# Kernel tuning notes

Measured on AMD Instinct MI355X. Metric: run time of the kernel, lower is better.

## Reference

```python
import jax, jax.numpy as jnp
import numpy as np

N, E = 50000, 500000          # nodes, edges
IN_DIM = 128
HID = 128
T, R, H, L = 4, 5, 4, 2       # node types, edge types, heads, layers
DK = HID // H                 # per-head dim


def setup_inputs() -> dict:
    key = jax.random.key(0)
    ks = jax.random.split(key, 16)
    s = 0.05
    inp = {
        "node_feature": jax.random.normal(ks[0], (N, IN_DIM), jnp.float32),
        "node_type": jax.random.randint(ks[1], (N,), 0, T, jnp.int32),
        "edge_time": jax.random.randint(ks[2], (E,), 0, 128, jnp.int32),
        "edge_index": jax.random.randint(ks[3], (2, E), 0, N, jnp.int32),
        "edge_type": jax.random.randint(ks[4], (E,), 0, R, jnp.int32),
        # per-node-type input adaptation
        "adapt_w": jax.random.normal(ks[5], (T, IN_DIM, HID), jnp.float32) * s,
        "adapt_b": jnp.zeros((T, HID), jnp.float32),
        # HGT layer params, stacked over layers L and node types T
        "kw": jax.random.normal(ks[6], (L, T, HID, HID), jnp.float32) * s,
        "kb": jnp.zeros((L, T, HID), jnp.float32),
        "qw": jax.random.normal(ks[7], (L, T, HID, HID), jnp.float32) * s,
        "qb": jnp.zeros((L, T, HID), jnp.float32),
        "vw": jax.random.normal(ks[8], (L, T, HID, HID), jnp.float32) * s,
        "vb": jnp.zeros((L, T, HID), jnp.float32),
        "aw": jax.random.normal(ks[9], (L, T, HID, HID), jnp.float32) * s,
        "ab": jnp.zeros((L, T, HID), jnp.float32),
        # relation (edge-type) specific params
        "rel_pri": jnp.ones((L, R, H), jnp.float32),
        "rel_att": jax.random.normal(ks[10], (L, R, H, DK, DK), jnp.float32) * (1.0 / np.sqrt(DK)),
        "rel_msg": jax.random.normal(ks[11], (L, R, H, DK, DK), jnp.float32) * (1.0 / np.sqrt(DK)),
        "skip": jnp.ones((L, T), jnp.float32),
    }
    return inp


def _type_linear(x, types, W, b):
    # per-node-type linear: small fixed loop over T types, masked select
    out = jnp.zeros((x.shape[0], W.shape[-1]), x.dtype)
    for t in range(W.shape[0]):
        out = jnp.where((types == t)[:, None], x @ W[t] + b[t], out)
    return out


def _hgt_layer(x, node_type, src, dst, edge_type,
               kw, kb, qw, qb, vw, vb, aw, ab, rel_pri, rel_att, rel_msg, skip):
    n = x.shape[0]
    k = _type_linear(x, node_type, kw, kb).reshape(n, H, DK)
    q = _type_linear(x, node_type, qw, qb).reshape(n, H, DK)
    v = _type_linear(x, node_type, vw, vb).reshape(n, H, DK)
    ke, qe, ve = k[src], q[dst], v[src]              # [E,H,DK] gathers
    att = jnp.zeros((ke.shape[0], H), x.dtype)
    msg = jnp.zeros_like(ve)
    inv_sqrt_dk = np.float32(1.0 / np.sqrt(DK))
    for r in range(R):                                # small fixed loop over edge types
        m = edge_type == r
        kt = jnp.einsum('ehi,hij->ehj', ke, rel_att[r])
        a = (qe * kt).sum(-1) * rel_pri[r] * inv_sqrt_dk   # [E,H]
        mt = jnp.einsum('ehi,hij->ehj', ve, rel_msg[r])    # [E,H,DK]
        att = jnp.where(m[:, None], a, att)
        msg = jnp.where(m[:, None, None], mt, msg)
    # segment softmax over incoming edges of each destination node
    amax = jax.ops.segment_max(att, dst, num_segments=n)
    amax = jnp.where(jnp.isfinite(amax), amax, 0.0)
    ex = jnp.exp(att - amax[dst])
    den = jax.ops.segment_sum(ex, dst, num_segments=n)
    alpha = ex / jnp.maximum(den[dst], 1e-9)
    res = jax.ops.segment_sum(alpha[:, :, None] * msg, dst, num_segments=n).reshape(n, HID)
    # target-specific update with gated residual (HGT skip)
    trans = _type_linear(jax.nn.gelu(res), node_type, aw, ab)
    sk = jax.nn.sigmoid(skip)[node_type][:, None]
    return trans * sk + x * (1.0 - sk)


def reference(node_feature, node_type, edge_time, edge_index, edge_type,
              adapt_w, adapt_b, kw, kb, qw, qb, vw, vb, aw, ab,
              rel_pri, rel_att, rel_msg, skip):
    # per-type adapt -> tanh (dropout p=0 is identity)
    h = jnp.tanh(_type_linear(node_feature, node_type, adapt_w, adapt_b))
    src, dst = edge_index[0], edge_index[1]
    for l in range(L):
        h = _hgt_layer(h, node_type, src, dst, edge_type,
                       kw[l], kb[l], qw[l], qb[l], vw[l], vb[l], aw[l], ab[l],
                       rel_pri[l], rel_att[l], rel_msg[l], skip[l])
    return h
```

## Files before the change

### kernel.cpp

```cpp
#include <hip/hip_runtime.h>

#define T_NT 4
#define T_R  5
#define T_H  4
#define T_DK 32
#define T_HD 128
#define T_L  2
#define NCOL 1408

typedef unsigned short u16;
typedef __bf16 bf8_t __attribute__((ext_vector_type(8)));
typedef float f4_t __attribute__((ext_vector_type(4)));

__device__ __forceinline__ float bf2f(u16 u){
  union { float f; unsigned int i; } v; v.i = ((unsigned int)u) << 16; return v.f;
}
__device__ __forceinline__ float blo(unsigned u){
  union { float f; unsigned int i; } v; v.i = u << 16; return v.f;
}
__device__ __forceinline__ float bhi(unsigned u){
  union { float f; unsigned int i; } v; v.i = u & 0xffff0000u; return v.f;
}
__device__ __forceinline__ u16 f2bf(float f){
  union { float f; unsigned int i; } v; v.f = f;
  unsigned int x = v.i;
  return (u16)((x + 0x7fffu + ((x >> 16) & 1u)) >> 16);
}
__device__ __forceinline__ unsigned pk2(float a, float b){
  return (unsigned)f2bf(a) | ((unsigned)f2bf(b) << 16);
}
__device__ __forceinline__ float gelu_f(float x){
  float x3 = x*x*x;
  return 0.5f * x * (1.f + tanhf(0.7978845608028654f * (x + 0.044715f * x3)));
}
__device__ __forceinline__ int perm_l(int m){
  return (m & ~31) | ((m & 4) << 2) | ((m & 24) >> 1) | (m & 3);
}

__global__ void k_hist4(const int* __restrict__ key, int* __restrict__ cnt, int n){
  __shared__ int c[T_NT];
  int tid = threadIdx.x;
  if (tid < T_NT) c[tid] = 0;
  __syncthreads();
  int base = blockIdx.x*1024;
#pragma unroll
  for (int j=0;j<4;j++){
    int i = base + tid + j*256;
    if (i < n) atomicAdd(&c[key[i]], 1);
  }
  __syncthreads();
  if (tid < T_NT) atomicAdd(&cnt[tid], c[tid]);
}

__global__ void k_toff(const int* __restrict__ cnt, int* __restrict__ off, int* __restrict__ tcur){
  if (threadIdx.x == 0){
    off[0] = 0;
    for (int t = 0; t < T_NT; ++t) off[t+1] = off[t] + cnt[t];
    for (int t = 0; t < T_NT; ++t) tcur[t] = off[t];
  }
}

__global__ void k_scatter2(const int* __restrict__ nt, int* __restrict__ tcur,
                           int* __restrict__ perm, int* __restrict__ iperm, int n){
  __shared__ int lc[T_NT], lb[T_NT];
  int tid = threadIdx.x;
  if (tid < T_NT) lc[tid] = 0;
  __syncthreads();
  int base = blockIdx.x*1024;
  int t[4], lr[4];
#pragma unroll
  for (int j=0;j<4;j++){
    int i = base + tid + j*256;
    if (i < n){ t[j] = nt[i]; lr[j] = atomicAdd(&lc[t[j]], 1); }
    else t[j] = -1;
  }
  __syncthreads();
  if (tid < T_NT) lb[tid] = atomicAdd(&tcur[tid], lc[tid]);
  __syncthreads();
#pragma unroll
  for (int j=0;j<4;j++){
    if (t[j] >= 0){
      int node = base + tid + j*256;
      int pos = lb[t[j]] + lr[j];
      perm[pos] = node;
      iperm[node] = pos;
    }
  }
}

__global__ void k_deg(const int* __restrict__ dstp, const int* __restrict__ iperm,
                      int* __restrict__ degp, int* __restrict__ rank, int n){
  int i = blockIdx.x*256 + threadIdx.x;
  if (i < n) rank[i] = atomicAdd(&degp[(size_t)iperm[dstp[i]] << 4], 1);
}

__global__ void k_scanA(const int* __restrict__ degp, int* __restrict__ rp,
                        int* __restrict__ bsum, int n){
  __shared__ int buf[256];
  int tid = threadIdx.x;
  int i = blockIdx.x*256 + tid;
  int v = (i < n) ? degp[(size_t)i << 4] : 0;
  buf[tid] = v;
  __syncthreads();
  for (int off = 1; off < 256; off <<= 1){
    int add = (tid >= off) ? buf[tid - off] : 0;
    __syncthreads();
    buf[tid] += add;
    __syncthreads();
  }
  if (i < n) rp[i] = buf[tid] - v;
  if (tid == 255) bsum[blockIdx.x] = buf[255];
}
__global__ void k_scanB(int* __restrict__ bsum, int nb){
  __shared__ int buf[1024];
  int tid = threadIdx.x;
  int v = (tid < nb) ? bsum[tid] : 0;
  buf[tid] = v;
  __syncthreads();
  for (int off = 1; off < 1024; off <<= 1){
    int add = (tid >= off) ? buf[tid - off] : 0;
    __syncthreads();
    buf[tid] += add;
    __syncthreads();
  }
  if (tid < nb) bsum[tid] = buf[tid] - v;
}
__global__ void k_scanC(int* __restrict__ rp, const int* __restrict__ bsum,
                        int n, int E){
  int i = blockIdx.x*256 + threadIdx.x;
  if (i < n) rp[i] += bsum[blockIdx.x];
  if (i == 0) rp[n] = E;
}

__global__ void k_fill2(const int* __restrict__ srcp, const int* __restrict__ dstp,
                        const int* __restrict__ etp, const int* __restrict__ iperm,
                        const int* __restrict__ rp, const int* __restrict__ rank,
                        int* __restrict__ packed, int n){
  int i = blockIdx.x*256 + threadIdx.x;
  if (i < n){
    int d = iperm[dstp[i]];
    packed[rp[d] + rank[i]] = iperm[srcp[i]] | (etp[i] << 17);
  }
}

__global__ void k_prepmisc(const float* __restrict__ kw, const float* __restrict__ kb,
                           const float* __restrict__ qb, const float* __restrict__ vb,
                           const float* __restrict__ rel_att, const float* __restrict__ rel_msg,
                           const float* __restrict__ rel_pri,
                           u16* __restrict__ Ball, float* __restrict__ biasall)
{
  const float isd = 0.17677669529663687f;
  int idx = blockIdx.x*256 + threadIdx.x;
  if (idx < T_L*T_NT*T_HD*T_HD){
    int col = idx & 127, k = (idx >> 7) & 127, lt = idx >> 14;
    Ball[((size_t)lt*NCOL + col)*T_HD + k] = f2bf(kw[((size_t)lt*T_HD + k)*T_HD + col]);
    if (k == 0) biasall[(size_t)lt*NCOL + col] = kb[(size_t)lt*T_HD + col];
    return;
  }
  int b = idx - T_L*T_NT*T_HD*T_HD;
  if (b >= T_L*T_NT*1280) return;
  int lt = b / 1280, cc = b % 1280;
  int l = lt >> 2;
  int qv = cc >= 640, rem = cc - qv*640;
  int r = rem >> 7, hd = rem & 127, h = hd >> 5, o = hd & 31;
  float s = 0.f;
  if (!qv){
    const float* Ar = rel_att + ((((size_t)l*T_R + r)*T_H + h)*T_DK + o)*T_DK;
    const float* qbr = qb + (size_t)lt*T_HD + h*T_DK;
#pragma unroll
    for (int j = 0; j < 32; ++j) s += qbr[j] * Ar[j];
    s *= rel_pri[((size_t)l*T_R + r)*T_H + h] * isd;
  } else {
    const float* Mr = rel_msg + (((size_t)l*T_R + r)*T_H + h)*T_DK*T_DK + o;
    const float* vbr = vb + (size_t)lt*T_HD + h*T_DK;
#pragma unroll
    for (int i = 0; i < 32; ++i) s += vbr[i] * Mr[i*T_DK];
  }
  biasall[(size_t)lt*NCOL + 128 + qv*640 + r*128 + h*32 + o] = s;
}

__global__ __launch_bounds__(256)
void k_prepqv(const float* __restrict__ qw, const float* __restrict__ vw,
              const float* __restrict__ rel_att, const float* __restrict__ rel_msg,
              const float* __restrict__ rel_pri, u16* __restrict__ Ball)
{
  __shared__ float Ws[T_HD*33];
  __shared__ float As_[T_R*32*36];
  const float isd = 0.17677669529663687f;
  int h = blockIdx.x & 3, qv = blockIdx.x >> 2;
  int t = blockIdx.y, l = blockIdx.z;
  int lt = l*T_NT + t;
  int tid = threadIdx.x;
  const float* W = (qv ? vw : qw) + (size_t)lt*T_HD*T_HD;
  const float* rel = (qv ? rel_msg : rel_att);
#pragma unroll
  for (int i = 0; i < 16; ++i){
    int idx = tid + i*256;
    int j = idx & 31, k = idx >> 5;
    Ws[k*33 + j] = W[(size_t)k*T_HD + h*T_DK + j];
  }
#pragma unroll
  for (int i = 0; i < 20; ++i){
    int idx = tid + i*256;
    int bcol = idx & 31, a = (idx >> 5) & 31, r = idx >> 10;
    float wv = rel[((((size_t)l*T_R + r)*T_H + h)*T_DK + a)*T_DK + bcol];
    if (qv) As_[r*1152 + bcol*36 + a] = wv;
    else    As_[r*1152 + a*36 + bcol] = wv;
  }
  __syncthreads();
  int k = tid & 127, io = tid >> 7;
  float Wrow[32];
#pragma unroll
  for (int c = 0; c < 32; ++c) Wrow[c] = Ws[k*33 + c];
  for (int r = 0; r < T_R; ++r){
    float scale = qv ? 1.f : rel_pri[((size_t)l*T_R + r)*T_H + h] * isd;
#pragma unroll
    for (int i2 = 0; i2 < 16; ++i2){
      int o = i2*2 + io;
      const float4* ap = (const float4*)&As_[r*1152 + o*36];
      float acc = 0.f;
#pragma unroll
      for (int c4 = 0; c4 < 8; ++c4){
        float4 a4 = ap[c4];
        acc += Wrow[c4*4+0]*a4.x + Wrow[c4*4+1]*a4.y + Wrow[c4*4+2]*a4.z + Wrow[c4*4+3]*a4.w;
      }
      int col = 128 + qv*640 + r*128 + h*32 + o;
      Ball[((size_t)lt*NCOL + col)*T_HD + k] = f2bf(acc*scale);
    }
  }
}

__global__ __launch_bounds__(256)
void k_qkvm(const float* __restrict__ X, const int* __restrict__ toff,
            const u16* __restrict__ Ball, const float* __restrict__ biasall,
            u16* __restrict__ kB, u16* __restrict__ qt, u16* __restrict__ mtp)
{
  __shared__ u16 As[64*128];
  int t = blockIdx.y;
  int z = blockIdx.z;
  int lo = toff[t], cnt = toff[t+1] - lo;
  int base = (int)blockIdx.x * 64;
  if (base >= cnt) return;
  int tid = threadIdx.x;
#pragma unroll
  for (int it = 0; it < 4; ++it){
    int chunk = tid + it*256;
    int row = chunk >> 4, c8 = (chunk & 15) << 3;
    uint4 o = make_uint4(0,0,0,0);
    if (base + row < cnt){
      const float* src = X + (size_t)(lo + base + row)*T_HD + c8;
      float4 f0 = *(const float4*)src;
      float4 f1 = *(const float4*)(src + 4);
      o.x = pk2(f0.x, f0.y);
      o.y = pk2(f0.z, f0.w);
      o.z = pk2(f1.x, f1.y);
      o.w = pk2(f1.z, f1.w);
    }
    int off16 = (row*128 + c8) ^ ((row & 7) << 3);
    *(uint4*)&As[off16] = o;
  }
  __syncthreads();

  int wid = tid >> 6, lane = tid & 63;
  int lr = lane & 15, lg = lane >> 4;
  bf8_t a[4][4];
#pragma unroll
  for (int rs = 0; rs < 4; ++rs)
#pragma unroll
    for (int kk = 0; kk < 4; ++kk){
      int row = rs*16 + lr;
      int off16 = (row*128 + kk*32 + lg*8) ^ ((row & 7) << 3);
      a[rs][kk] = *(const bf8_t*)&As[off16];
    }

  const u16* Bt = Ball + (size_t)t * NCOL * T_HD;
  const float* biast = biasall + (size_t)t * NCOL;

  int ci_end = z ? 44 : 22;
  for (int ci = z*22 + wid; ci < ci_end; ci += 4){
    int c0 = ci*2;
    int col0 = c0*16 + lr;
    const u16* bp0 = Bt + (size_t)col0*T_HD + lg*8;
    const u16* bp1 = bp0 + (size_t)16*T_HD;
    bf8_t b00 = *(const bf8_t*)(bp0);
    bf8_t b01 = *(const bf8_t*)(bp0 + 32);
    bf8_t b02 = *(const bf8_t*)(bp0 + 64);
    bf8_t b03 = *(const bf8_t*)(bp0 + 96);
    bf8_t b10 = *(const bf8_t*)(bp1);
    bf8_t b11 = *(const bf8_t*)(bp1 + 32);
    bf8_t b12 = *(const bf8_t*)(bp1 + 64);
    bf8_t b13 = *(const bf8_t*)(bp1 + 96);
    f4_t acc0[4], acc1[4];
#pragma unroll
    for (int rs = 0; rs < 4; ++rs){ acc0[rs] = (f4_t){0.f,0.f,0.f,0.f}; acc1[rs] = (f4_t){0.f,0.f,0.f,0.f}; }
#pragma unroll
    for (int rs = 0; rs < 4; ++rs){
      acc0[rs] = __builtin_amdgcn_mfma_f32_16x16x32_bf16(b00, a[rs][0], acc0[rs], 0, 0, 0);
      acc0[rs] = __builtin_amdgcn_mfma_f32_16x16x32_bf16(b01, a[rs][1], acc0[rs], 0, 0, 0);
      acc0[rs] = __builtin_amdgcn_mfma_f32_16x16x32_bf16(b02, a[rs][2], acc0[rs], 0, 0, 0);
      acc0[rs] = __builtin_amdgcn_mfma_f32_16x16x32_bf16(b03, a[rs][3], acc0[rs], 0, 0, 0);
      acc1[rs] = __builtin_amdgcn_mfma_f32_16x16x32_bf16(b10, a[rs][0], acc1[rs], 0, 0, 0);
      acc1[rs] = __builtin_amdgcn_mfma_f32_16x16x32_bf16(b11, a[rs][1], acc1[rs], 0, 0, 0);
      acc1[rs] = __builtin_amdgcn_mfma_f32_16x16x32_bf16(b12, a[rs][2], acc1[rs], 0, 0, 0);
      acc1[rs] = __builtin_amdgcn_mfma_f32_16x16x32_bf16(b13, a[rs][3], acc1[rs], 0, 0, 0);
    }
    float4 bias0 = *(const float4*)&biast[c0*16 + lg*4];
    float4 bias1 = *(const float4*)&biast[c0*16 + 16 + lg*4];
    int mco = ci*32 + lg*8;
    u16* dst; int cofs, stride;
    if (ci < 4)       { dst = kB;  cofs = mco;        stride = T_HD; }
    else if (ci < 24) { dst = qt;  cofs = mco - 128;  stride = T_R*T_HD; }
    else              { dst = mtp; cofs = mco - 768;  stride = T_R*T_HD; }
#pragma unroll
    for (int rs = 0; rs < 4; ++rs){
      int nl = rs*16 + lr;
      if (base + nl < cnt){
        uint4 o;
        o.x = pk2(acc0[rs][0] + bias0.x, acc0[rs][1] + bias0.y);
        o.y = pk2(acc0[rs][2] + bias0.z, acc0[rs][3] + bias0.w);
        o.z = pk2(acc1[rs][0] + bias1.x, acc1[rs][1] + bias1.y);
        o.w = pk2(acc1[rs][2] + bias1.z, acc1[rs][3] + bias1.w);
        *(uint4*)&dst[(size_t)(lo + base + nl)*stride + cofs] = o;
      }
    }
  }
}

template<int MODE, int GIN, int SOUT>
__global__ __launch_bounds__(256)
void k_typed_gemm(const float* __restrict__ X,
                  const int* __restrict__ tperm, const int* __restrict__ toff,
                  const float* __restrict__ W, const float* __restrict__ Bi,
                  float* __restrict__ outv,
                  const float* __restrict__ h_in, const float* __restrict__ skipv)
{
  int t = blockIdx.y;
  int lo = toff[t], cnt = toff[t+1] - lo;
  int base = (int)blockIdx.x * 64;
  if (base >= cnt) return;
  __shared__ float As[64][16];
  __shared__ float Bs[16][128];
  __shared__ int rows_s[64];
  int tid = threadIdx.x;
  if (GIN || SOUT){
    if (tid < 64) rows_s[tid] = (base + tid < cnt) ? tperm[lo + base + tid] : -1;
    __syncthreads();
  }
  float acc[8][4];
#pragma unroll
  for (int i=0;i<8;i++){ acc[i][0]=0.f;acc[i][1]=0.f;acc[i][2]=0.f;acc[i][3]=0.f; }
  int ty = tid >> 5, tx = tid & 31;
  const float* Wt = W + (size_t)t * (T_HD*T_HD);
  for (int k0 = 0; k0 < T_HD; k0 += 16){
#pragma unroll
    for (int j=0;j<4;j++){
      int idx = tid + j*256;
      int m = idx >> 4, kk = idx & 15;
      float v = 0.f;
      if (base + m < cnt){
        if (GIN){
          int row = rows_s[m];
          v = X[(size_t)row*T_HD + k0 + kk];
        } else {
          v = X[(size_t)(lo + base + m)*T_HD + k0 + kk];
        }
        if (MODE == 3) v = gelu_f(v);
      }
      As[m][kk] = v;
    }
#pragma unroll
    for (int j=0;j<8;j++){
      int idx = tid + j*256;
      int kk = idx >> 7, c = idx & 127;
      int kg = k0 + kk;
      if (MODE == 3) kg = perm_l(kg);
      Bs[kk][c] = Wt[(size_t)kg*T_HD + c];
    }
    __syncthreads();
#pragma unroll
    for (int kk=0;kk<16;kk++){
      float4 bv = *(const float4*)&Bs[kk][tx*4];
#pragma unroll
      for (int i=0;i<8;i++){
        float a = As[ty*8+i][kk];
        acc[i][0] += a*bv.x; acc[i][1] += a*bv.y; acc[i][2] += a*bv.z; acc[i][3] += a*bv.w;
      }
    }
    __syncthreads();
  }
  float sk = 0.f;
  if (MODE == 3) sk = 1.f / (1.f + __expf(-skipv[t]));
#pragma unroll
  for (int i=0;i<8;i++){
    int m = ty*8 + i;
    if (base + m >= cnt) continue;
    size_t opos = SOUT ? (size_t)rows_s[m] : (size_t)(lo + base + m);
#pragma unroll
    for (int q=0;q<4;q++){
      int c = tx*4 + q;
      float vv = acc[i][q] + Bi[t*T_HD + c];
      if (MODE == 1) vv = tanhf(vv);
      if (MODE == 3) vv = vv*sk + h_in[(size_t)(lo + base + m)*T_HD + c]*(1.f - sk);
      outv[opos*T_HD + c] = vv;
    }
  }
}

__global__ __launch_bounds__(256)
void k_edge_attn2(const u16* __restrict__ kB, const u16* __restrict__ qt,
                  const u16* __restrict__ mtp, const int* __restrict__ rp,
                  const int* __restrict__ packed, float* __restrict__ resb, int n)
{
  int lane = threadIdx.x & 63;
  int wid = (int)blockIdx.x * (blockDim.x >> 6) + (threadIdx.x >> 6);
  int nw = (int)gridDim.x * (blockDim.x >> 6);
  int l2 = lane << 1;
  for (int dst = wid; dst < n; dst += nw){
    int e0 = rp[dst], e1 = rp[dst+1];
    if (e0 == e1){
      *(float2*)&resb[(size_t)dst*T_HD + l2] = make_float2(0.f, 0.f);
      continue;
    }
    const u16* qrow = qt + (size_t)dst*(T_R*T_HD) + l2;
    float mA=-INFINITY, dA=0.f, aA0=0.f, aA1=0.f;
    float mB=-INFINITY, dB=0.f, aB0=0.f, aB1=0.f;
    int ei = e0;
    for (; ei + 1 < e1; ei += 2){
      int pka = packed[ei], pkb = packed[ei+1];
      int sa = pka & 131071, ra = pka >> 17;
      int sb = pkb & 131071, rb = pkb >> 17;
      unsigned ka = *(const unsigned*)&kB[(sa << 7) + l2];
      unsigned kb = *(const unsigned*)&kB[(sb << 7) + l2];
      unsigned qa = *(const unsigned*)&qrow[ra << 7];
      unsigned qb = *(const unsigned*)&qrow[rb << 7];
      unsigned ma = *(const unsigned*)&mtp[((sa*T_R + ra) << 7) + l2];
      unsigned mb = *(const unsigned*)&mtp[((sb*T_R + rb) << 7) + l2];
      float pa = blo(qa)*blo(ka) + bhi(qa)*bhi(ka);
      float pb = blo(qb)*blo(kb) + bhi(qb)*bhi(kb);
      pa += __shfl_xor(pa, 1);  pb += __shfl_xor(pb, 1);
      pa += __shfl_xor(pa, 2);  pb += __shfl_xor(pb, 2);
      pa += __shfl_xor(pa, 4);  pb += __shfl_xor(pb, 4);
      pa += __shfl_xor(pa, 8);  pb += __shfl_xor(pb, 8);
      float mnA = fmaxf(mA, pa), mnB = fmaxf(mB, pb);
      float scA = __expf(mA - mnA), scB = __expf(mB - mnB);
      float wA = __expf(pa - mnA),  wB = __expf(pb - mnB);
      mA = mnA; mB = mnB;
      dA  = dA*scA + wA;          dB  = dB*scB + wB;
      aA0 = aA0*scA + wA*blo(ma); aB0 = aB0*scB + wB*blo(mb);
      aA1 = aA1*scA + wA*bhi(ma); aB1 = aB1*scB + wB*bhi(mb);
    }
    if (ei < e1){
      int pka = packed[ei];
      int sa = pka & 131071, ra = pka >> 17;
      unsigned ka = *(const unsigned*)&kB[(sa << 7) + l2];
      unsigned qa = *(const unsigned*)&qrow[ra << 7];
      unsigned ma = *(const unsigned*)&mtp[((sa*T_R + ra) << 7) + l2];
      float pa = blo(qa)*blo(ka) + bhi(qa)*bhi(ka);
      pa += __shfl_xor(pa, 1);
      pa += __shfl_xor(pa, 2);
      pa += __shfl_xor(pa, 4);
      pa += __shfl_xor(pa, 8);
      float mnA = fmaxf(mA, pa);
      float scA = __expf(mA - mnA);
      float wA = __expf(pa - mnA);
      mA = mnA;
      dA  = dA*scA + wA;
      aA0 = aA0*scA + wA*blo(ma);
      aA1 = aA1*scA + wA*bhi(ma);
    }
    float mn = fmaxf(mA, mB);
    float eA = __expf(mA - mn), eB = __expf(mB - mn);
    float d  = dA*eA + dB*eB;
    float a0 = aA0*eA + aB0*eB;
    float a1 = aA1*eA + aB1*eB;
    float inv = 1.f / fmaxf(d, 1e-9f);
    *(float2*)&resb[(size_t)dst*T_HD + l2] = make_float2(a0*inv, a1*inv);
  }
}

extern "C" void kernel_launch(void* const* d_in, const int* in_sizes, int n_in,
                              void* d_out, int out_size, void* d_ws, size_t ws_size,
                              hipStream_t stream)
{
  const float* node_feature = (const float*)d_in[0];
  const int* node_type    = (const int*)d_in[1];
  const int* edge_index   = (const int*)d_in[3];
  const int* edge_type    = (const int*)d_in[4];
  const float* adapt_w = (const float*)d_in[5];
  const float* adapt_b = (const float*)d_in[6];
  const float* kw = (const float*)d_in[7];
  const float* kb = (const float*)d_in[8];
  const float* qw = (const float*)d_in[9];
  const float* qb = (const float*)d_in[10];
  const float* vw = (const float*)d_in[11];
  const float* vb = (const float*)d_in[12];
  const float* aw = (const float*)d_in[13];
  const float* ab = (const float*)d_in[14];
  const float* rel_pri = (const float*)d_in[15];
  const float* rel_att = (const float*)d_in[16];
  const float* rel_msg = (const float*)d_in[17];
  const float* skipp   = (const float*)d_in[18];

  const int N = in_sizes[1];
  const int E = in_sizes[4];
  const int* srcp = edge_index;
  const int* dstp = edge_index + E;

  char* p = (char*)d_ws;
  auto take = [&](size_t bytes)->char*{
    char* r = p; p += (bytes + 255) & ~(size_t)255; return r;
  };
  float* h0   = (float*)take((size_t)N*T_HD*4);
  float* resb = (float*)take((size_t)N*T_HD*4);
  u16*  kB    = (u16*) take((size_t)N*T_HD*2);
  u16*  qt    = (u16*) take((size_t)N*T_R*T_HD*2);
  u16*  mtp   = (u16*) take((size_t)N*T_R*T_HD*2);
  u16*  Ball  = (u16*) take((size_t)T_L*T_NT*NCOL*T_HD*2);
  float* biasall = (float*)take((size_t)T_L*T_NT*NCOL*4);
  int* degp   = (int*) take((size_t)N*16*4);
  int* rp     = (int*) take(((size_t)N+1)*4);
  int* rank   = (int*) take((size_t)E*4);
  int* packed = (int*) take((size_t)E*4);
  int* tcnt   = (int*) take(256);
  int* toff   = (int*) take(256);
  int* tcur   = (int*) take(256);
  int* bsum   = (int*) take(1024);
  int* tperm  = (int*) take((size_t)N*4);
  int* iperm  = (int*) take((size_t)N*4);

  hipMemsetAsync(degp, 0, (size_t)N*16*4, stream);
  hipMemsetAsync(tcnt, 0, 256, stream);

  int nb_n4 = (N + 1023)/1024, nb_e = (E + 255)/256;
  int nb_s  = (N + 255)/256;
  k_hist4<<<nb_n4, 256, 0, stream>>>(node_type, tcnt, N);
  k_toff<<<1, 64, 0, stream>>>(tcnt, toff, tcur);
  k_scatter2<<<nb_n4, 256, 0, stream>>>(node_type, tcur, tperm, iperm, N);
  k_deg<<<nb_e, 256, 0, stream>>>(dstp, iperm, degp, rank, E);
  k_scanA<<<nb_s, 256, 0, stream>>>(degp, rp, bsum, N);
  k_scanB<<<1, 1024, 0, stream>>>(bsum, nb_s);
  k_scanC<<<nb_s, 256, 0, stream>>>(rp, bsum, N, E);
  k_fill2<<<nb_e, 256, 0, stream>>>(srcp, dstp, edge_type, iperm, rp, rank, packed, E);

  int misc_total = T_L*T_NT*T_HD*T_HD + T_L*T_NT*1280;
  k_prepmisc<<<(misc_total + 255)/256, 256, 0, stream>>>(
      kw, kb, qb, vb, rel_att, rel_msg, rel_pri, Ball, biasall);
  k_prepqv<<<dim3(8, T_NT, T_L), 256, 0, stream>>>(
      qw, vw, rel_att, rel_msg, rel_pri, Ball);

  dim3 gg((N + 63)/64, T_NT);
  dim3 gq((N + 63)/64, T_NT, 2);
  k_typed_gemm<1,1,0><<<gg, 256, 0, stream>>>(node_feature, tperm, toff, adapt_w, adapt_b, h0, nullptr, nullptr);

  for (int l = 0; l < T_L; ++l){
    size_t wo = (size_t)l * T_NT * T_HD * T_HD;
    size_t bo = (size_t)l * T_NT * T_HD;
    k_qkvm<<<gq, 256, 0, stream>>>(h0, toff,
        Ball + (size_t)l*T_NT*NCOL*T_HD, biasall + (size_t)l*T_NT*NCOL,
        kB, qt, mtp);
    k_edge_attn2<<<2048, 256, 0, stream>>>(kB, qt, mtp, rp, packed, resb, N);
    if (l == T_L - 1)
      k_typed_gemm<3,0,1><<<gg, 256, 0, stream>>>(resb, tperm, toff, aw+wo, ab+bo,
          (float*)d_out, h0, skipp + l*T_NT);
    else
      k_typed_gemm<3,0,0><<<gg, 256, 0, stream>>>(resb, tperm, toff, aw+wo, ab+bo,
          h0, h0, skipp + l*T_NT);
  }
}
```

Before: 460.6 us.

## Replace fp32 typed GEMMs with bf16 MFMA kernels using pre-transposed weights

The per-type adapt and output GEMMs move from scalar fp32 shared-memory tiling to bf16 MFMA 16x16x32 instructions. A new prep kernel converts adapt_w and aw to transposed bf16 and folds the row permutation into the aw copy. The activation tile is staged once in swizzled LDS as bf16, so the k-loop and its barriers disappear. This cuts FMA issue cost on three small GEMMs but lowers input and weight precision to bf16 and adds one prep launch.

```diff
diff --git a/kernel.cpp b/kernel.cpp
--- a/kernel.cpp
+++ b/kernel.cpp
@@ -227,6 +227,21 @@
       int col = 128 + qv*640 + r*128 + h*32 + o;
       Ball[((size_t)lt*NCOL + col)*T_HD + k] = f2bf(acc*scale);
     }
+  }
+}
+
+__global__ void k_prepw2(const float* __restrict__ adapt_w, const float* __restrict__ aw,
+                         u16* __restrict__ adaptT, u16* __restrict__ awT)
+{
+  int idx = blockIdx.x*256 + threadIdx.x;
+  if (idx < T_NT*T_HD*T_HD){
+    int k = idx & 127, col = (idx >> 7) & 127, t = idx >> 14;
+    adaptT[idx] = f2bf(adapt_w[((size_t)t*T_HD + k)*T_HD + col]);
+  } else {
+    int j = idx - T_NT*T_HD*T_HD;
+    if (j >= T_L*T_NT*T_HD*T_HD) return;
+    int k = j & 127, col = (j >> 7) & 127, lt = j >> 14;
+    awT[j] = f2bf(aw[((size_t)lt*T_HD + perm_l(k))*T_HD + col]);
   }
 }
 
@@ -328,80 +343,103 @@
 
 template<int MODE, int GIN, int SOUT>
 __global__ __launch_bounds__(256)
-void k_typed_gemm(const float* __restrict__ X,
-                  const int* __restrict__ tperm, const int* __restrict__ toff,
-                  const float* __restrict__ W, const float* __restrict__ Bi,
-                  float* __restrict__ outv,
-                  const float* __restrict__ h_in, const float* __restrict__ skipv)
+void k_ffn(const float* __restrict__ X, const int* __restrict__ tperm,
+           const int* __restrict__ toff, const u16* __restrict__ WT,
+           const float* __restrict__ Bi, float* __restrict__ outv,
+           const float* __restrict__ h_in, const float* __restrict__ skipv)
 {
+  __shared__ u16 As[64*128];
+  __shared__ int rows_s[64];
   int t = blockIdx.y;
   int lo = toff[t], cnt = toff[t+1] - lo;
   int base = (int)blockIdx.x * 64;
   if (base >= cnt) return;
-  __shared__ float As[64][16];
-  __shared__ float Bs[16][128];
-  __shared__ int rows_s[64];
   int tid = threadIdx.x;
   if (GIN || SOUT){
-    if (tid < 64) rows_s[tid] = (base + tid < cnt) ? tperm[lo + base + tid] : -1;
+    if (tid < 64) rows_s[tid] = (base + tid < cnt) ? tperm[lo + base + tid] : 0;
     __syncthreads();
   }
-  float acc[8][4];
-#pragma unroll
-  for (int i=0;i<8;i++){ acc[i][0]=0.f;acc[i][1]=0.f;acc[i][2]=0.f;acc[i][3]=0.f; }
-  int ty = tid >> 5, tx = tid & 31;
-  const float* Wt = W + (size_t)t * (T_HD*T_HD);
-  for (int k0 = 0; k0 < T_HD; k0 += 16){
-#pragma unroll
-    for (int j=0;j<4;j++){
-      int idx = tid + j*256;
-      int m = idx >> 4, kk = idx & 15;
-      float v = 0.f;
-      if (base + m < cnt){
-        if (GIN){
-          int row = rows_s[m];
-          v = X[(size_t)row*T_HD + k0 + kk];
-        } else {
-          v = X[(size_t)(lo + base + m)*T_HD + k0 + kk];
-        }
-        if (MODE == 3) v = gelu_f(v);
+#pragma unroll
+  for (int it = 0; it < 4; ++it){
+    int chunk = tid + it*256;
+    int row = chunk >> 4, c8 = (chunk & 15) << 3;
+    uint4 o = make_uint4(0,0,0,0);
+    if (base + row < cnt){
+      const float* src = GIN ? (X + (size_t)rows_s[row]*T_HD + c8)
+                             : (X + (size_t)(lo + base + row)*T_HD + c8);
+      float4 f0 = *(const float4*)src;
+      float4 f1 = *(const float4*)(src + 4);
+      if (MODE == 3){
+        f0.x = gelu_f(f0.x); f0.y = gelu_f(f0.y); f0.z = gelu_f(f0.z); f0.w = gelu_f(f0.w);
+        f1.x = gelu_f(f1.x); f1.y = gelu_f(f1.y); f1.z = gelu_f(f1.z); f1.w = gelu_f(f1.w);
       }
-      As[m][kk] = v;
-    }
-#pragma unroll
-    for (int j=0;j<8;j++){
-      int idx = tid + j*256;
-      int kk = idx >> 7, c = idx & 127;
-      int kg = k0 + kk;
-      if (MODE == 3) kg = perm_l(kg);
-      Bs[kk][c] = Wt[(size_t)kg*T_HD + c];
-    }
-    __syncthreads();
-#pragma unroll
-    for (int kk=0;kk<16;kk++){
-      float4 bv = *(const float4*)&Bs[kk][tx*4];
-#pragma unroll
-      for (int i=0;i<8;i++){
-        float a = As[ty*8+i][kk];
-        acc[i][0] += a*bv.x; acc[i][1] += a*bv.y; acc[i][2] += a*bv.z; acc[i][3] += a*bv.w;
-      }
-    }
-    __syncthreads();
-  }
+      o.x = pk2(f0.x, f0.y);
+      o.y = pk2(f0.z, f0.w);
+      o.z = pk2(f1.x, f1.y);
+      o.w = pk2(f1.z, f1.w);
+    }
+    int off16 = (row*128 + c8) ^ ((row & 7) << 3);
+    *(uint4*)&As[off16] = o;
+  }
+  __syncthreads();
+
+  int wid = tid >> 6, lane = tid & 63;
+  int lr = lane & 15, lg = lane >> 4;
+  bf8_t a[4][4];
+#pragma unroll
+  for (int rs = 0; rs < 4; ++rs)
+#pragma unroll
+    for (int kk = 0; kk < 4; ++kk){
+      int row = rs*16 + lr;
+      int off16 = (row*128 + kk*32 + lg*8) ^ ((row & 7) << 3);
+      a[rs][kk] = *(const bf8_t*)&As[off16];
+    }
+
+  const u16* Wt = WT + (size_t)t * T_HD * T_HD;
   float sk = 0.f;
   if (MODE == 3) sk = 1.f / (1.f + __expf(-skipv[t]));
-#pragma unroll
-  for (int i=0;i<8;i++){
-    int m = ty*8 + i;
-    if (base + m >= cnt) continue;
-    size_t opos = SOUT ? (size_t)rows_s[m] : (size_t)(lo + base + m);
-#pragma unroll
-    for (int q=0;q<4;q++){
-      int c = tx*4 + q;
-      float vv = acc[i][q] + Bi[t*T_HD + c];
-      if (MODE == 1) vv = tanhf(vv);
-      if (MODE == 3) vv = vv*sk + h_in[(size_t)(lo + base + m)*T_HD + c]*(1.f - sk);
-      outv[opos*T_HD + c] = vv;
+
+  for (int c = wid; c < 8; c += 4){
+    const u16* bp = Wt + (size_t)(c*16 + lr)*T_HD + lg*8;
+    bf8_t b0 = *(const bf8_t*)(bp);
+    bf8_t b1 = *(const bf8_t*)(bp + 32);
+    bf8_t b2 = *(const bf8_t*)(bp + 64);
+    bf8_t b3 = *(const bf8_t*)(bp + 96);
+    f4_t acc[4];
+#pragma unroll
+    for (int rs = 0; rs < 4; ++rs) acc[rs] = (f4_t){0.f,0.f,0.f,0.f};
+#pragma unroll
+    for (int rs = 0; rs < 4; ++rs){
+      acc[rs] = __builtin_amdgcn_mfma_f32_16x16x32_bf16(b0, a[rs][0], acc[rs], 0, 0, 0);
+      acc[rs] = __builtin_amdgcn_mfma_f32_16x16x32_bf16(b1, a[rs][1], acc[rs], 0, 0, 0);
+      acc[rs] = __builtin_amdgcn_mfma_f32_16x16x32_bf16(b2, a[rs][2], acc[rs], 0, 0, 0);
+      acc[rs] = __builtin_amdgcn_mfma_f32_16x16x32_bf16(b3, a[rs][3], acc[rs], 0, 0, 0);
+    }
+    int cc = c*16 + lg*4;
+    float4 bias4 = *(const float4*)&Bi[t*T_HD + cc];
+#pragma unroll
+    for (int rs = 0; rs < 4; ++rs){
+      int nl = rs*16 + lr;
+      if (base + nl < cnt){
+        float4 vv;
+        vv.x = acc[rs][0] + bias4.x;
+        vv.y = acc[rs][1] + bias4.y;
+        vv.z = acc[rs][2] + bias4.z;
+        vv.w = acc[rs][3] + bias4.w;
+        if (MODE == 1){
+          vv.x = tanhf(vv.x); vv.y = tanhf(vv.y); vv.z = tanhf(vv.z); vv.w = tanhf(vv.w);
+        }
+        if (MODE == 3){
+          float4 hr = *(const float4*)&h_in[(size_t)(lo + base + nl)*T_HD + cc];
+          float osk = 1.f - sk;
+          vv.x = vv.x*sk + hr.x*osk;
+          vv.y = vv.y*sk + hr.y*osk;
+          vv.z = vv.z*sk + hr.z*osk;
+          vv.w = vv.w*sk + hr.w*osk;
+        }
+        size_t opos = SOUT ? (size_t)rows_s[nl] : (size_t)(lo + base + nl);
+        *(float4*)&outv[opos*T_HD + cc] = vv;
+      }
     }
   }
 }
@@ -517,6 +555,8 @@
   u16*  mtp   = (u16*) take((size_t)N*T_R*T_HD*2);
   u16*  Ball  = (u16*) take((size_t)T_L*T_NT*NCOL*T_HD*2);
   float* biasall = (float*)take((size_t)T_L*T_NT*NCOL*4);
+  u16*  adaptT = (u16*)take((size_t)T_NT*T_HD*T_HD*2);
+  u16*  awT    = (u16*)take((size_t)T_L*T_NT*T_HD*T_HD*2);
   int* degp   = (int*) take((size_t)N*16*4);
   int* rp     = (int*) take(((size_t)N+1)*4);
   int* rank   = (int*) take((size_t)E*4);
@@ -547,23 +587,24 @@
       kw, kb, qb, vb, rel_att, rel_msg, rel_pri, Ball, biasall);
   k_prepqv<<<dim3(8, T_NT, T_L), 256, 0, stream>>>(
       qw, vw, rel_att, rel_msg, rel_pri, Ball);
+  int w2_total = T_NT*T_HD*T_HD + T_L*T_NT*T_HD*T_HD;
+  k_prepw2<<<(w2_total + 255)/256, 256, 0, stream>>>(adapt_w, aw, adaptT, awT);
 
   dim3 gg((N + 63)/64, T_NT);
   dim3 gq((N + 63)/64, T_NT, 2);
-  k_typed_gemm<1,1,0><<<gg, 256, 0, stream>>>(node_feature, tperm, toff, adapt_w, adapt_b, h0, nullptr, nullptr);
+  k_ffn<1,1,0><<<gg, 256, 0, stream>>>(node_feature, tperm, toff, adaptT, adapt_b, h0, nullptr, nullptr);
 
   for (int l = 0; l < T_L; ++l){
-    size_t wo = (size_t)l * T_NT * T_HD * T_HD;
     size_t bo = (size_t)l * T_NT * T_HD;
     k_qkvm<<<gq, 256, 0, stream>>>(h0, toff,
         Ball + (size_t)l*T_NT*NCOL*T_HD, biasall + (size_t)l*T_NT*NCOL,
         kB, qt, mtp);
     k_edge_attn2<<<2048, 256, 0, stream>>>(kB, qt, mtp, rp, packed, resb, N);
     if (l == T_L - 1)
-      k_typed_gemm<3,0,1><<<gg, 256, 0, stream>>>(resb, tperm, toff, aw+wo, ab+bo,
-          (float*)d_out, h0, skipp + l*T_NT);
+      k_ffn<3,0,1><<<gg, 256, 0, stream>>>(resb, tperm, toff,
+          awT + (size_t)l*T_NT*T_HD*T_HD, ab + bo, (float*)d_out, h0, skipp + l*T_NT);
     else
-      k_typed_gemm<3,0,0><<<gg, 256, 0, stream>>>(resb, tperm, toff, aw+wo, ab+bo,
-          h0, h0, skipp + l*T_NT);
-  }
-}
+      k_ffn<3,0,0><<<gg, 256, 0, stream>>>(resb, tperm, toff,
+          awT + (size_t)l*T_NT*T_HD*T_HD, ab + bo, h0, h0, skipp + l*T_NT);
+  }
+}
```

Result: faster. 392.9 us (-14.7%).
